# Performance work log

Measured on AMD Instinct MI355X. Metric: run time of the kernel, lower is better.

The kernel has to match this reference:

```python
import jax, jax.numpy as jnp
import numpy as np

DIM = 1024
HID = 2 * DIM
NUM_EXPERTS = 8
TOP_K = 2
BATCH, SEQ = 2, 2048


def setup_inputs() -> dict:
    key = jax.random.key(0)
    ks = jax.random.split(key, 8)
    s = 0.02
    return {
        "x": jax.random.normal(ks[0], (BATCH, SEQ, DIM), jnp.float32),
        "router_w": jax.random.normal(ks[1], (DIM, NUM_EXPERTS), jnp.float32) * s,
        "router_b": jnp.zeros((NUM_EXPERTS,), jnp.float32),
        "sw1": jax.random.normal(ks[2], (DIM, HID), jnp.float32) * s,
        "sb1": jnp.zeros((HID,), jnp.float32),
        "sw2": jax.random.normal(ks[3], (HID, DIM), jnp.float32) * s,
        "sb2": jnp.zeros((DIM,), jnp.float32),
        "ew1": jax.random.normal(ks[4], (NUM_EXPERTS, DIM, HID), jnp.float32) * s,
        "eb1": jnp.zeros((NUM_EXPERTS, HID), jnp.float32),
        "ew2": jax.random.normal(ks[5], (NUM_EXPERTS, HID, DIM), jnp.float32) * s,
        "eb2": jnp.zeros((NUM_EXPERTS, DIM), jnp.float32),
    }


def _gelu(x):
    # torch nn.GELU default is the exact (erf) form
    return jax.nn.gelu(x, approximate=False)


def reference(x, router_w, router_b, sw1, sb1, sw2, sb2, ew1, eb1, ew2, eb2):
    B, S, D = x.shape
    flat = x.reshape(-1, D)                      # [T, D]
    T = flat.shape[0]

    # Router: softmax -> top-k -> renormalize
    probs = jax.nn.softmax(flat @ router_w + router_b, axis=-1)  # [T, E]
    top_w, top_i = jax.lax.top_k(probs, TOP_K)                   # [T, K]
    top_w = top_w / jnp.sum(top_w, axis=-1, keepdims=True)
    # Dense per-token combine weights [T, E] (zero for unrouted experts)
    comb = jnp.zeros_like(probs).at[jnp.arange(T)[:, None], top_i].set(top_w)

    # Shared expert (always on)
    shared = _gelu(flat @ sw1 + sb1) @ sw2 + sb2                 # [T, D]

    # All experts as one batched GEMM pair; zero weights kill unrouted tokens.
    h = _gelu(jnp.einsum('td,edh->eth', flat, ew1) + eb1[:, None, :])  # [E, T, H]
    eo = jnp.einsum('eth,ehd->etd', h, ew2) + eb2[:, None, :]          # [E, T, D]
    moe = jnp.einsum('te,etd->td', comb, eo)                           # [T, D]

    return (shared + moe).reshape(B, S, D)
```

## Files before the change

kernel.cpp:

```cpp
#include <hip/hip_runtime.h>

#define DIM   1024
#define HID   2048
#define NE    8
#define T_TOK 4096

typedef __attribute__((ext_vector_type(8))) short short8;
typedef __attribute__((ext_vector_type(4))) float f32x4;

__device__ __forceinline__ ushort f2bf(float f) {
    union { float f; unsigned u; } v; v.f = f;
    unsigned r = v.u + 0x7FFFu + ((v.u >> 16) & 1u);
    return (ushort)(r >> 16);
}

__device__ __forceinline__ float gelu_exact(float x) {
    return 0.5f * x * (1.0f + erff(x * 0.70710678118654752f));
}

__global__ void convert_x(const float* __restrict__ in, ushort* __restrict__ out, int n8) {
    int i = blockIdx.x * blockDim.x + threadIdx.x;
    if (i >= n8) return;
    const float4* p = (const float4*)in + (size_t)i * 2;
    float4 a = p[0], b = p[1];
    short8 o;
    o[0] = (short)f2bf(a.x); o[1] = (short)f2bf(a.y);
    o[2] = (short)f2bf(a.z); o[3] = (short)f2bf(a.w);
    o[4] = (short)f2bf(b.x); o[5] = (short)f2bf(b.y);
    o[6] = (short)f2bf(b.z); o[7] = (short)f2bf(b.w);
    *(short8*)(out + (size_t)i * 8) = o;
}

__global__ void transpose_conv9(const float* __restrict__ ew, const float* __restrict__ sw,
                                ushort* __restrict__ ewT, ushort* __restrict__ swT,
                                int R, int C) {
    __shared__ float tile[32][65];
    int z = blockIdx.z;
    const float* in = (z < NE) ? ew + (size_t)z * R * C : sw;
    ushort* out     = (z < NE) ? ewT + (size_t)z * R * C : swT;
    int c0 = blockIdx.x * 32, r0 = blockIdx.y * 64;
    int tx = threadIdx.x & 31, ty = threadIdx.x >> 5;
#pragma unroll
    for (int rr = 0; rr < 64; rr += 8)
        tile[tx][rr + ty] = in[(size_t)(r0 + rr + ty) * C + (c0 + tx)];
    __syncthreads();
    int lane = threadIdx.x & 63, q = threadIdx.x >> 6;
#pragma unroll
    for (int j = 0; j < 8; ++j) {
        int cc = q * 8 + j;
        out[(size_t)(c0 + cc) * R + (r0 + lane)] = f2bf(tile[cc][lane]);
    }
}

__global__ void router_kernel(const float* __restrict__ x, const float* __restrict__ rw,
                              const float* __restrict__ rb, int* __restrict__ cnt,
                              int* __restrict__ ids, float* __restrict__ wts) {
    int wave = threadIdx.x >> 6;
    int lane = threadIdx.x & 63;
    int t = blockIdx.x * 4 + wave;
    const float* xr = x + (size_t)t * DIM;
    float acc[NE];
#pragma unroll
    for (int e = 0; e < NE; ++e) acc[e] = 0.f;
    for (int d = lane; d < DIM; d += 64) {
        float xv = xr[d];
#pragma unroll
        for (int e = 0; e < NE; ++e) acc[e] += xv * rw[d * NE + e];
    }
#pragma unroll
    for (int e = 0; e < NE; ++e) {
#pragma unroll
        for (int off = 32; off; off >>= 1) acc[e] += __shfl_xor(acc[e], off);
    }
    if (lane == 0) {
        float l[NE];
#pragma unroll
        for (int e = 0; e < NE; ++e) l[e] = acc[e] + rb[e];
        int i1 = 0;
#pragma unroll
        for (int e = 1; e < NE; ++e) if (l[e] > l[i1]) i1 = e;
        int i2 = (i1 == 0) ? 1 : 0;
#pragma unroll
        for (int e = 0; e < NE; ++e) if (e != i1 && l[e] > l[i2]) i2 = e;
        float p2 = __expf(l[i2] - l[i1]);
        float w1 = 1.0f / (1.0f + p2);
        float w2 = p2 / (1.0f + p2);
        int pos1 = atomicAdd(&cnt[i1], 1);
        ids[i1 * T_TOK + pos1] = t; wts[i1 * T_TOK + pos1] = w1;
        int pos2 = atomicAdd(&cnt[i2], 1);
        ids[i2 * T_TOK + pos2] = t; wts[i2 * T_TOK + pos2] = w2;
    }
}

__global__ void build_queue(const int* __restrict__ cnt, int* __restrict__ offs,
                            int* __restrict__ q1, int* __restrict__ n1,
                            int* __restrict__ q2, int* __restrict__ n2) {
    if (threadIdx.x != 0) return;
    int s = 0;
    for (int e = 0; e < NE; ++e) { offs[e] = s; s += cnt[e]; }
    int k1 = 0, k2 = 0;
    for (int z = 0; z <= NE; ++z) {
        int c = (z < NE) ? cnt[z] : T_TOK;
        int mts = (c + 255) >> 8;
        for (int mt = 0; mt < mts; ++mt) {
            for (int nt = 0; nt < HID / 256; ++nt)
                q1[k1++] = (z << 16) | (mt << 8) | nt;
            for (int nt = 0; nt < DIM / 256; ++nt)
                q2[k2++] = (z << 16) | (mt << 8) | nt;
        }
    }
    *n1 = k1; *n2 = k2;
}

__device__ __forceinline__ void mma256(
    const ushort* __restrict__ A, const int* __restrict__ gather, int count,
    const ushort* __restrict__ BT, int K, int tileM, int tileN,
    ushort* lds, f32x4 acc[8][4])
{
    const int tid  = threadIdx.x;
    const int lane = tid & 63, wave = tid >> 6;
    const int wr = wave >> 2, wc = wave & 3;
    const int g = lane >> 4, fr = lane & 15;
    const int swl = (fr & 7) << 3;
    const int sub = lane >> 3;
    const int kcs = ((lane & 7) ^ sub) << 3;

    const ushort* asrc[4];
    const ushort* bsrc[4];
#pragma unroll
    for (int i = 0; i < 4; ++i) {
        int row = (wave * 4 + i) * 8 + sub;
        int ar = tileM + row; if (ar > count - 1) ar = count - 1;
        int grow = gather ? gather[ar] : ar;
        asrc[i] = A  + (size_t)grow * K + kcs;
        bsrc[i] = BT + (size_t)(tileN + row) * K + kcs;
    }

    auto STAGE = [&](int buf, int t) {
        ushort* base = lds + buf * 32768;
#pragma unroll
        for (int i = 0; i < 4; ++i) {
            int chunk = wave * 4 + i;
            __builtin_amdgcn_global_load_lds(
                (const __attribute__((address_space(1))) void*)(asrc[i] + t * 64),
                (__attribute__((address_space(3))) void*)(base + chunk * 512),
                16, 0, 0);
            __builtin_amdgcn_global_load_lds(
                (const __attribute__((address_space(1))) void*)(bsrc[i] + t * 64),
                (__attribute__((address_space(3))) void*)(base + 16384 + chunk * 512),
                16, 0, 0);
        }
    };

    auto COMPUTE = [&](int buf) {
        const ushort* A_s = lds + buf * 32768;
        const ushort* B_s = A_s + 16384;
#pragma unroll
        for (int kk = 0; kk < 2; ++kk) {
            int koff = (kk * 32 + g * 8) ^ swl;
            short8 a[8], b[4];
#pragma unroll
            for (int m = 0; m < 8; ++m) {
                int row = wr * 128 + m * 16 + fr;
                a[m] = *(const short8*)&A_s[row * 64 + koff];
            }
#pragma unroll
            for (int n = 0; n < 4; ++n) {
                int col = wc * 64 + n * 16 + fr;
                b[n] = *(const short8*)&B_s[col * 64 + koff];
            }
#pragma unroll
            for (int m = 0; m < 8; ++m)
#pragma unroll
                for (int n = 0; n < 4; ++n)
                    acc[m][n] = __builtin_amdgcn_mfma_f32_16x16x32_bf16(
                        a[m], b[n], acc[m][n], 0, 0, 0);
        }
    };

    const int NT = K >> 6;
    STAGE(0, 0);
    for (int t = 0; t < NT; ++t) {
        int cur = t & 1;
        if (t + 1 < NT) {
            STAGE(cur ^ 1, t + 1);
            asm volatile("s_waitcnt vmcnt(8)" ::: "memory");
        } else {
            asm volatile("s_waitcnt vmcnt(0)" ::: "memory");
        }
        __builtin_amdgcn_s_barrier();
        asm volatile("" ::: "memory");
        COMPUTE(cur);
        asm volatile("" ::: "memory");
        __builtin_amdgcn_s_barrier();
    }
}

__global__ __launch_bounds__(512, 2)
void gemm1_kernel(const ushort* __restrict__ xb,
                  const ushort* __restrict__ ew1T, const ushort* __restrict__ sw1T,
                  const float* __restrict__ eb1, const float* __restrict__ sb1,
                  const int* __restrict__ ids, const int* __restrict__ cnt,
                  const int* __restrict__ offs,
                  const int* __restrict__ q1, const int* __restrict__ n1,
                  ushort* __restrict__ h)
{
    extern __shared__ ushort lds[];
    const int nit = *n1;
    const int lane = threadIdx.x & 63, wave = threadIdx.x >> 6;
    const int wr = wave >> 2, wc = wave & 3, g = lane >> 4, fr = lane & 15;

    for (int it = blockIdx.x; it < nit; it += gridDim.x) {
        int item = q1[it];
        int z = item >> 16, mt = (item >> 8) & 255, nt = item & 255;
        int count, hbase;
        const ushort* BT; const float* bias; const int* gather;
        if (z < NE) {
            count  = cnt[z];
            BT     = ew1T + (size_t)z * HID * DIM;
            bias   = eb1 + z * HID;
            gather = ids + z * T_TOK;
            hbase  = T_TOK + offs[z];
        } else {
            count = T_TOK; BT = sw1T; bias = sb1; gather = nullptr; hbase = 0;
        }
        int tileM = mt * 256, tileN = nt * 256;

        f32x4 acc[8][4];
#pragma unroll
        for (int m = 0; m < 8; ++m)
#pragma unroll
            for (int n = 0; n < 4; ++n) acc[m][n] = (f32x4){0.f, 0.f, 0.f, 0.f};

        mma256(xb, gather, count, BT, DIM, tileM, tileN, lds, acc);

#pragma unroll
        for (int n = 0; n < 4; ++n) {
            int col = tileN + wc * 64 + n * 16 + fr;
            float bc = bias[col];
#pragma unroll
            for (int m = 0; m < 8; ++m) {
#pragma unroll
                for (int i = 0; i < 4; ++i) {
                    int row = tileM + wr * 128 + m * 16 + g * 4 + i;
                    if (row < count)
                        h[(size_t)(hbase + row) * HID + col] =
                            f2bf(gelu_exact(acc[m][n][i] + bc));
                }
            }
        }
        __syncthreads();
    }
}

__global__ __launch_bounds__(512, 2)
void gemm2_kernel(const ushort* __restrict__ h,
                  const ushort* __restrict__ ew2T, const ushort* __restrict__ sw2T,
                  const float* __restrict__ eb2, const float* __restrict__ sb2,
                  const int* __restrict__ ids, const float* __restrict__ wts,
                  const int* __restrict__ cnt, const int* __restrict__ offs,
                  const int* __restrict__ q2, const int* __restrict__ n2,
                  float* __restrict__ out)
{
    extern __shared__ ushort lds[];
    const int nit = *n2;
    const int lane = threadIdx.x & 63, wave = threadIdx.x >> 6;
    const int wr = wave >> 2, wc = wave & 3, g = lane >> 4, fr = lane & 15;

    for (int it = blockIdx.x; it < nit; it += gridDim.x) {
        int item = q2[it];
        int z = item >> 16, mt = (item >> 8) & 255, nt = item & 255;
        int count;
        const ushort* BT; const float* bias; const int* toks; const float* tw;
        const ushort* Arows;
        if (z < NE) {
            count = cnt[z];
            BT    = ew2T + (size_t)z * DIM * HID;
            bias  = eb2 + z * DIM;
            toks  = ids + z * T_TOK;
            tw    = wts + z * T_TOK;
            Arows = h + (size_t)(T_TOK + offs[z]) * HID;
        } else {
            count = T_TOK; BT = sw2T; bias = sb2; toks = nullptr; tw = nullptr;
            Arows = h;
        }
        int tileM = mt * 256, tileN = nt * 256;

        f32x4 acc[8][4];
#pragma unroll
        for (int m = 0; m < 8; ++m)
#pragma unroll
            for (int n = 0; n < 4; ++n) acc[m][n] = (f32x4){0.f, 0.f, 0.f, 0.f};

        mma256(Arows, nullptr, count, BT, HID, tileM, tileN, lds, acc);

#pragma unroll
        for (int n = 0; n < 4; ++n) {
            int col = tileN + wc * 64 + n * 16 + fr;
            float bc = bias[col];
#pragma unroll
            for (int m = 0; m < 8; ++m) {
#pragma unroll
                for (int i = 0; i < 4; ++i) {
                    int row = tileM + wr * 128 + m * 16 + g * 4 + i;
                    if (row < count) {
                        int token = toks ? toks[row] : row;
                        float w   = tw ? tw[row] : 1.0f;
                        atomicAdd(out + (size_t)token * DIM + col, w * (acc[m][n][i] + bc));
                    }
                }
            }
        }
        __syncthreads();
    }
}

extern "C" void kernel_launch(void* const* d_in, const int* in_sizes, int n_in,
                              void* d_out, int out_size, void* d_ws, size_t ws_size,
                              hipStream_t stream)
{
    const float* x   = (const float*)d_in[0];
    const float* rw  = (const float*)d_in[1];
    const float* rb  = (const float*)d_in[2];
    const float* sw1 = (const float*)d_in[3];
    const float* sb1 = (const float*)d_in[4];
    const float* sw2 = (const float*)d_in[5];
    const float* sb2 = (const float*)d_in[6];
    const float* ew1 = (const float*)d_in[7];
    const float* eb1 = (const float*)d_in[8];
    const float* ew2 = (const float*)d_in[9];
    const float* eb2 = (const float*)d_in[10];
    float* out = (float*)d_out;

    char* p = (char*)d_ws;
    ushort* xb   = (ushort*)p;  p += (size_t)T_TOK * DIM * 2;
    ushort* sw1T = (ushort*)p;  p += (size_t)HID * DIM * 2;
    ushort* sw2T = (ushort*)p;  p += (size_t)DIM * HID * 2;
    ushort* ew1T = (ushort*)p;  p += (size_t)NE * HID * DIM * 2;
    ushort* ew2T = (ushort*)p;  p += (size_t)NE * DIM * HID * 2;
    ushort* hbuf = (ushort*)p;  p += (size_t)(3 * T_TOK) * HID * 2;
    int*    ids  = (int*)p;     p += (size_t)NE * T_TOK * 4;
    float*  wts  = (float*)p;   p += (size_t)NE * T_TOK * 4;
    int*    cnt  = (int*)p;     p += 256;
    int*    offs = (int*)p;     p += 256;
    int*    q1   = (int*)p;     p += 4608;
    int*    q2   = (int*)p;     p += 2304;
    int*    nq   = (int*)p;     p += 256;

    hipFuncSetAttribute((const void*)gemm1_kernel,
                        hipFuncAttributeMaxDynamicSharedMemorySize, 131072);
    hipFuncSetAttribute((const void*)gemm2_kernel,
                        hipFuncAttributeMaxDynamicSharedMemorySize, 131072);

    hipMemsetAsync(cnt, 0, 256, stream);
    hipMemsetAsync(out, 0, (size_t)out_size * 4, stream);

    convert_x<<<dim3((T_TOK * DIM / 8 + 255) / 256), 256, 0, stream>>>(x, xb, T_TOK * DIM / 8);
    transpose_conv9<<<dim3(HID / 32, DIM / 64, NE + 1), 256, 0, stream>>>(
        ew1, sw1, ew1T, sw1T, DIM, HID);
    transpose_conv9<<<dim3(DIM / 32, HID / 64, NE + 1), 256, 0, stream>>>(
        ew2, sw2, ew2T, sw2T, HID, DIM);
    router_kernel<<<dim3(T_TOK / 4), 256, 0, stream>>>(x, rw, rb, cnt, ids, wts);
    build_queue<<<dim3(1), 64, 0, stream>>>(cnt, offs, q1, nq, q2, nq + 1);
    gemm1_kernel<<<dim3(256), 512, 131072, stream>>>(
        xb, ew1T, sw1T, eb1, sb1, ids, cnt, offs, q1, nq, hbuf);
    gemm2_kernel<<<dim3(256), 512, 131072, stream>>>(
        hbuf, ew2T, sw2T, eb2, sb2, ids, wts, cnt, offs, q2, nq + 1, out);
}
```

Before: 416.5 us.

## Replace atomic scatter with slot stores plus combine kernel, fuse x conversion

```diff
diff --git a/kernel.cpp b/kernel.cpp
--- a/kernel.cpp
+++ b/kernel.cpp
@@ -14,21 +14,11 @@
     return (ushort)(r >> 16);
 }
 
-__device__ __forceinline__ float gelu_exact(float x) {
-    return 0.5f * x * (1.0f + erff(x * 0.70710678118654752f));
-}
-
-__global__ void convert_x(const float* __restrict__ in, ushort* __restrict__ out, int n8) {
-    int i = blockIdx.x * blockDim.x + threadIdx.x;
-    if (i >= n8) return;
-    const float4* p = (const float4*)in + (size_t)i * 2;
-    float4 a = p[0], b = p[1];
-    short8 o;
-    o[0] = (short)f2bf(a.x); o[1] = (short)f2bf(a.y);
-    o[2] = (short)f2bf(a.z); o[3] = (short)f2bf(a.w);
-    o[4] = (short)f2bf(b.x); o[5] = (short)f2bf(b.y);
-    o[6] = (short)f2bf(b.z); o[7] = (short)f2bf(b.w);
-    *(short8*)(out + (size_t)i * 8) = o;
+__device__ __forceinline__ float gelu_fast(float x) {
+    float t = x * x;
+    float u = x * (1.0f + 0.044715f * t);
+    float e = exp2f(2.3020585f * u);
+    return x - x / (e + 1.0f);
 }
 
 __global__ void transpose_conv9(const float* __restrict__ ew, const float* __restrict__ sw,
@@ -54,18 +44,35 @@
 
 __global__ void router_kernel(const float* __restrict__ x, const float* __restrict__ rw,
                               const float* __restrict__ rb, int* __restrict__ cnt,
-                              int* __restrict__ ids, float* __restrict__ wts) {
+                              int* __restrict__ ids, float* __restrict__ wts,
+                              int* __restrict__ te, int* __restrict__ tp,
+                              ushort* __restrict__ xb) {
     int wave = threadIdx.x >> 6;
     int lane = threadIdx.x & 63;
     int t = blockIdx.x * 4 + wave;
     const float* xr = x + (size_t)t * DIM;
+    ushort* xo = xb + (size_t)t * DIM;
     float acc[NE];
 #pragma unroll
     for (int e = 0; e < NE; ++e) acc[e] = 0.f;
-    for (int d = lane; d < DIM; d += 64) {
-        float xv = xr[d];
-#pragma unroll
-        for (int e = 0; e < NE; ++e) acc[e] += xv * rw[d * NE + e];
+    {
+        int d0 = lane * 16;
+        float v[16];
+#pragma unroll
+        for (int j = 0; j < 16; j += 4) {
+            float4 f = *(const float4*)(xr + d0 + j);
+            v[j] = f.x; v[j+1] = f.y; v[j+2] = f.z; v[j+3] = f.w;
+        }
+        short8 o0, o1;
+#pragma unroll
+        for (int j = 0; j < 8; ++j) { o0[j] = (short)f2bf(v[j]); o1[j] = (short)f2bf(v[8+j]); }
+        *(short8*)(xo + d0)     = o0;
+        *(short8*)(xo + d0 + 8) = o1;
+#pragma unroll
+        for (int j = 0; j < 16; ++j) {
+#pragma unroll
+            for (int e = 0; e < NE; ++e) acc[e] += v[j] * rw[(d0 + j) * NE + e];
+        }
     }
 #pragma unroll
     for (int e = 0; e < NE; ++e) {
@@ -87,8 +94,10 @@
         float w2 = p2 / (1.0f + p2);
         int pos1 = atomicAdd(&cnt[i1], 1);
         ids[i1 * T_TOK + pos1] = t; wts[i1 * T_TOK + pos1] = w1;
+        te[2 * t] = i1; tp[2 * t] = pos1;
         int pos2 = atomicAdd(&cnt[i2], 1);
         ids[i2 * T_TOK + pos2] = t; wts[i2 * T_TOK + pos2] = w2;
+        te[2 * t + 1] = i2; tp[2 * t + 1] = pos2;
     }
 }
 
@@ -245,7 +254,7 @@
                     int row = tileM + wr * 128 + m * 16 + g * 4 + i;
                     if (row < count)
                         h[(size_t)(hbase + row) * HID + col] =
-                            f2bf(gelu_exact(acc[m][n][i] + bc));
+                            f2bf(gelu_fast(acc[m][n][i] + bc));
                 }
             }
         }
@@ -257,10 +266,10 @@
 void gemm2_kernel(const ushort* __restrict__ h,
                   const ushort* __restrict__ ew2T, const ushort* __restrict__ sw2T,
                   const float* __restrict__ eb2, const float* __restrict__ sb2,
-                  const int* __restrict__ ids, const float* __restrict__ wts,
+                  const float* __restrict__ wts,
                   const int* __restrict__ cnt, const int* __restrict__ offs,
                   const int* __restrict__ q2, const int* __restrict__ n2,
-                  float* __restrict__ out)
+                  float* __restrict__ eo, float* __restrict__ out)
 {
     extern __shared__ ushort lds[];
     const int nit = *n2;
@@ -271,18 +280,19 @@
         int item = q2[it];
         int z = item >> 16, mt = (item >> 8) & 255, nt = item & 255;
         int count;
-        const ushort* BT; const float* bias; const int* toks; const float* tw;
+        const ushort* BT; const float* bias; const float* tw; float* dst;
         const ushort* Arows;
         if (z < NE) {
             count = cnt[z];
             BT    = ew2T + (size_t)z * DIM * HID;
             bias  = eb2 + z * DIM;
-            toks  = ids + z * T_TOK;
             tw    = wts + z * T_TOK;
             Arows = h + (size_t)(T_TOK + offs[z]) * HID;
+            dst   = eo + (size_t)offs[z] * DIM;
         } else {
-            count = T_TOK; BT = sw2T; bias = sb2; toks = nullptr; tw = nullptr;
+            count = T_TOK; BT = sw2T; bias = sb2; tw = nullptr;
             Arows = h;
+            dst   = out;
         }
         int tileM = mt * 256, tileN = nt * 256;
 
@@ -295,24 +305,37 @@
         mma256(Arows, nullptr, count, BT, HID, tileM, tileN, lds, acc);
 
 #pragma unroll
-        for (int n = 0; n < 4; ++n) {
-            int col = tileN + wc * 64 + n * 16 + fr;
-            float bc = bias[col];
-#pragma unroll
-            for (int m = 0; m < 8; ++m) {
-#pragma unroll
-                for (int i = 0; i < 4; ++i) {
-                    int row = tileM + wr * 128 + m * 16 + g * 4 + i;
-                    if (row < count) {
-                        int token = toks ? toks[row] : row;
-                        float w   = tw ? tw[row] : 1.0f;
-                        atomicAdd(out + (size_t)token * DIM + col, w * (acc[m][n][i] + bc));
+        for (int m = 0; m < 8; ++m) {
+#pragma unroll
+            for (int i = 0; i < 4; ++i) {
+                int row = tileM + wr * 128 + m * 16 + g * 4 + i;
+                if (row < count) {
+                    float w = tw ? tw[row] : 1.0f;
+#pragma unroll
+                    for (int n = 0; n < 4; ++n) {
+                        int col = tileN + wc * 64 + n * 16 + fr;
+                        dst[(size_t)row * DIM + col] = w * (acc[m][n][i] + bias[col]);
                     }
                 }
             }
         }
         __syncthreads();
     }
+}
+
+__global__ void combine_kernel(const float* __restrict__ eo, const int* __restrict__ te,
+                               const int* __restrict__ tp, const int* __restrict__ offs,
+                               float* __restrict__ out)
+{
+    int t = blockIdx.x;
+    int s1 = offs[te[2 * t]]     + tp[2 * t];
+    int s2 = offs[te[2 * t + 1]] + tp[2 * t + 1];
+    int d = threadIdx.x * 4;
+    float4 a = *(const float4*)(out + (size_t)t * DIM + d);
+    float4 b = *(const float4*)(eo + (size_t)s1 * DIM + d);
+    float4 c = *(const float4*)(eo + (size_t)s2 * DIM + d);
+    a.x += b.x + c.x; a.y += b.y + c.y; a.z += b.z + c.z; a.w += b.w + c.w;
+    *(float4*)(out + (size_t)t * DIM + d) = a;
 }
 
 extern "C" void kernel_launch(void* const* d_in, const int* in_sizes, int n_in,
@@ -339,8 +362,11 @@
     ushort* ew1T = (ushort*)p;  p += (size_t)NE * HID * DIM * 2;
     ushort* ew2T = (ushort*)p;  p += (size_t)NE * DIM * HID * 2;
     ushort* hbuf = (ushort*)p;  p += (size_t)(3 * T_TOK) * HID * 2;
+    float*  eo   = (float*)p;   p += (size_t)(2 * T_TOK) * DIM * 4;
     int*    ids  = (int*)p;     p += (size_t)NE * T_TOK * 4;
     float*  wts  = (float*)p;   p += (size_t)NE * T_TOK * 4;
+    int*    te   = (int*)p;     p += (size_t)2 * T_TOK * 4;
+    int*    tp   = (int*)p;     p += (size_t)2 * T_TOK * 4;
     int*    cnt  = (int*)p;     p += 256;
     int*    offs = (int*)p;     p += 256;
     int*    q1   = (int*)p;     p += 4608;
@@ -353,17 +379,16 @@
                         hipFuncAttributeMaxDynamicSharedMemorySize, 131072);
 
     hipMemsetAsync(cnt, 0, 256, stream);
-    hipMemsetAsync(out, 0, (size_t)out_size * 4, stream);
-
-    convert_x<<<dim3((T_TOK * DIM / 8 + 255) / 256), 256, 0, stream>>>(x, xb, T_TOK * DIM / 8);
+
+    router_kernel<<<dim3(T_TOK / 4), 256, 0, stream>>>(x, rw, rb, cnt, ids, wts, te, tp, xb);
     transpose_conv9<<<dim3(HID / 32, DIM / 64, NE + 1), 256, 0, stream>>>(
         ew1, sw1, ew1T, sw1T, DIM, HID);
     transpose_conv9<<<dim3(DIM / 32, HID / 64, NE + 1), 256, 0, stream>>>(
         ew2, sw2, ew2T, sw2T, HID, DIM);
-    router_kernel<<<dim3(T_TOK / 4), 256, 0, stream>>>(x, rw, rb, cnt, ids, wts);
     build_queue<<<dim3(1), 64, 0, stream>>>(cnt, offs, q1, nq, q2, nq + 1);
     gemm1_kernel<<<dim3(256), 512, 131072, stream>>>(
         xb, ew1T, sw1T, eb1, sb1, ids, cnt, offs, q1, nq, hbuf);
     gemm2_kernel<<<dim3(256), 512, 131072, stream>>>(
-        hbuf, ew2T, sw2T, eb2, sb2, ids, wts, cnt, offs, q2, nq + 1, out);
-}
+        hbuf, ew2T, sw2T, eb2, sb2, wts, cnt, offs, q2, nq + 1, eo, out);
+    combine_kernel<<<dim3(T_TOK), 256, 0, stream>>>(eo, te, tp, offs, out);
+}
```

After: 348.4 us. -16.4%, faster.
